# Kernel tuning notes

Measured on AMD Instinct MI355X. Metric: run time of the kernel, lower is better.

## Reference

```python
import jax, jax.numpy as jnp
import numpy as np

WH, WW = 7, 7
N = WH * WW
DIM = 384
HEADS = 12
NW = 64          # windows per image
B_ = 2048        # batch * NW


def _relative_position_index():
    ch, cw = np.meshgrid(np.arange(WH), np.arange(WW), indexing='ij')
    coords = np.stack([ch, cw]).reshape(2, -1)                      # [2, N]
    rel = coords[:, :, None] - coords[:, None, :]                   # [2, N, N]
    rel = rel.transpose(1, 2, 0)
    rel[:, :, 0] += WH - 1
    rel[:, :, 1] += WW - 1
    rel[:, :, 0] *= 2 * WW - 1
    return jnp.asarray(rel.sum(-1), dtype=jnp.int32)                # [N, N]


def setup_inputs() -> dict:
    key = jax.random.key(0)
    ks = jax.random.split(key, 7)
    return {
        'x': jax.random.normal(ks[0], (B_, N, DIM), dtype=jnp.float32),
        'qkv_w': jax.random.normal(ks[1], (3 * DIM, DIM), dtype=jnp.float32) * 0.02,
        'qkv_b': jax.random.normal(ks[2], (3 * DIM,), dtype=jnp.float32) * 0.02,
        'proj_w': jax.random.normal(ks[3], (DIM, DIM), dtype=jnp.float32) * 0.02,
        'proj_b': jax.random.normal(ks[4], (DIM,), dtype=jnp.float32) * 0.02,
        'bias_table': jax.random.normal(ks[5], ((2 * WH - 1) * (2 * WW - 1), HEADS), dtype=jnp.float32) * 0.02,
        'mask': jax.random.normal(ks[6], (NW, N, N), dtype=jnp.float32),
        'rel_idx': _relative_position_index(),
    }


def reference(x, qkv_w, qkv_b, proj_w, proj_b, bias_table, mask, rel_idx):
    B_, n, C = x.shape
    H = HEADS
    hd = C // H
    scale = hd ** (-0.5)

    qkv = x @ qkv_w.T + qkv_b                                        # [B_, N, 3C]
    qkv = qkv.reshape(B_, n, 3, H, hd).transpose(2, 0, 3, 1, 4)      # [3, B_, H, N, hd]
    q, k, v = qkv[0], qkv[1], qkv[2]

    attn = jnp.einsum('bhqd,bhkd->bhqk', q * scale, k)               # [B_, H, N, N]

    rpb = bias_table[rel_idx.reshape(-1)].reshape(n, n, H)           # gather [N, N, H]
    attn = attn + rpb.transpose(2, 0, 1)[None]                       # [B_, H, N, N]

    nW = mask.shape[0]
    attn = attn.reshape(B_ // nW, nW, H, n, n) + mask[None, :, None]
    attn = attn.reshape(B_, H, n, n)
    attn = jax.nn.softmax(attn, axis=-1)

    out = jnp.einsum('bhqk,bhkd->bhqd', attn, v)                     # [B_, H, N, hd]
    out = out.transpose(0, 2, 1, 3).reshape(B_, n, C)
    return out @ proj_w.T + proj_b
```

## Files before the change

kernel.cpp:

```cpp
#include <hip/hip_runtime.h>
#include <hip/hip_bf16.h>
#include <cstdint>
#include <cstddef>

#define NTOK 49
#define DIM 384
#define KDIM 384
#define HEADS 12
#define HD 32
#define BATCH 2048
#define MROWS (BATCH * NTOK)

typedef unsigned short u16;
typedef __bf16 bf16x8 __attribute__((ext_vector_type(8)));
typedef unsigned short u16x8 __attribute__((ext_vector_type(8)));
typedef float f32x4 __attribute__((ext_vector_type(4)));

__device__ __forceinline__ u16 f2b(float f) {
  union { float f; unsigned u; } v; v.f = f;
  unsigned r = v.u + 0x7fffu + ((v.u >> 16) & 1u);
  return (u16)(r >> 16);
}

__device__ __forceinline__ bf16x8 ld_bf8(const u16* p) {
  u16x8 u = *(const u16x8*)p;
  return __builtin_bit_cast(bf16x8, u);
}

__device__ __forceinline__ void gload_lds16(const void* g, void* l) {
  __builtin_amdgcn_global_load_lds(
      (const __attribute__((address_space(1))) unsigned*)g,
      (__attribute__((address_space(3))) unsigned*)l, 16, 0, 0);
}

__global__ __launch_bounds__(256) void k_prep(const float* __restrict__ x,
                                              u16* __restrict__ xb,
                                              const float* __restrict__ qkv_w,
                                              u16* __restrict__ wqkvb,
                                              const float* __restrict__ proj_w,
                                              u16* __restrict__ wprojb,
                                              const float* __restrict__ bias_table,
                                              const float* __restrict__ mask,
                                              const int* __restrict__ rel_idx,
                                              float* __restrict__ rpbm) {
  int blk = blockIdx.x;
  if (blk < 38208) {
    const float* in;
    u16* out;
    int i;
    if (blk < 37632) {
      in = x; out = xb; i = blk * 256 + threadIdx.x;
    } else if (blk < 38064) {
      in = qkv_w; out = wqkvb; i = (blk - 37632) * 256 + threadIdx.x;
    } else {
      in = proj_w; out = wprojb; i = (blk - 38064) * 256 + threadIdx.x;
    }
    float4 v = ((const float4*)in)[i];
    ushort4 o;
    o.x = f2b(v.x); o.y = f2b(v.y); o.z = f2b(v.z); o.w = f2b(v.w);
    ((ushort4*)out)[i] = o;
  } else {
    int idx = (blk - 38208) * 256 + threadIdx.x;
    int r  = idx & 3;
    int l  = (idx >> 2) & 63;
    int ni = (idx >> 8) & 3;
    int mi = (idx >> 10) & 3;
    int w  = (idx >> 12) & 63;
    int h  = idx >> 18;
    int row = mi * 16 + (l >> 4) * 4 + r;
    int col = ni * 16 + (l & 15);
    float v = -1e30f;
    if (row < NTOK && col < NTOK)
      v = bias_table[rel_idx[row * NTOK + col] * HEADS + h] +
          mask[(w * NTOK + row) * NTOK + col];
    rpbm[idx] = v;
  }
}

template <int OUT_BF16, int NCOLS, int NTN, int GD8>
__global__ __launch_bounds__(256) void k_gemm(const u16* __restrict__ A,
                                              const u16* __restrict__ B,
                                              const float* __restrict__ bias,
                                              void* __restrict__ Cv) {
  __shared__ u16 sh[24576];
  int bid = blockIdx.x;
  int tile = (bid & 7) * GD8 + (bid >> 3);
  int mt = tile / NTN, nt = tile - mt * NTN;
  long m0 = (long)mt * 128;
  int n0 = nt * 128;
  int tid = threadIdx.x;
  int lane = tid & 63, wid = tid >> 6;
  int wr = (wid >> 1) * 64, wc = (wid & 1) * 64;
  int c = lane & 15, g = lane >> 4;
  int gsw = (g ^ ((c >> 1) & 3)) * 8;

  int srow = wid * 16 + (lane >> 2);
  int scol = ((lane & 3) ^ ((lane >> 3) & 3)) * 8;
  const u16* gA = A + (m0 + srow) * (long)KDIM + scol;
  const u16* gB = B + (long)(n0 + srow) * KDIM + scol;
  int lrow = srow, lseg = (lane & 3) * 8;

  f32x4 acc[4][4] = {};

#define STAGE(BUF, KT)                                                         \
  {                                                                            \
    u16* As_ = sh + (BUF) * 8192;                                              \
    u16* Bs_ = As_ + 4096;                                                     \
    gload_lds16(gA + (KT), &As_[lrow * 32 + lseg]);                            \
    gload_lds16(gA + (KT) + 64L * KDIM, &As_[(lrow + 64) * 32 + lseg]);        \
    gload_lds16(gB + (KT), &Bs_[lrow * 32 + lseg]);                            \
    gload_lds16(gB + (KT) + 64L * KDIM, &Bs_[(lrow + 64) * 32 + lseg]);        \
  }

#define GITER(T, NV)                                                           \
  {                                                                            \
    asm volatile("s_waitcnt vmcnt(" #NV ")" ::: "memory");                     \
    __builtin_amdgcn_s_barrier();                                              \
    const u16* As = sh + ((T) % 3) * 8192;                                     \
    const u16* Bs = As + 4096;                                                 \
    bf16x8 af[4], bfr[4];                                                      \
    _Pragma("unroll") for (int i = 0; i < 4; ++i) {                            \
      af[i]  = ld_bf8(&As[(wr + i * 16 + c) * 32 + gsw]);                      \
      bfr[i] = ld_bf8(&Bs[(wc + i * 16 + c) * 32 + gsw]);                      \
    }                                                                          \
    asm volatile("s_waitcnt lgkmcnt(0)" ::: "memory");                         \
    __builtin_amdgcn_s_barrier();                                              \
    if ((T) + 3 < 12) STAGE((T) % 3, ((T) + 3) * 32);                          \
    __builtin_amdgcn_s_setprio(1);                                             \
    _Pragma("unroll") for (int mi = 0; mi < 4; ++mi)                           \
    _Pragma("unroll") for (int ni = 0; ni < 4; ++ni)                           \
        acc[mi][ni] = __builtin_amdgcn_mfma_f32_16x16x32_bf16(                 \
            af[mi], bfr[ni], acc[mi][ni], 0, 0, 0);                            \
    __builtin_amdgcn_s_setprio(0);                                             \
  }

  STAGE(0, 0);
  STAGE(1, 32);
  STAGE(2, 64);
  GITER(0, 8)  GITER(1, 8)  GITER(2, 8)  GITER(3, 8)
  GITER(4, 8)  GITER(5, 8)  GITER(6, 8)  GITER(7, 8)
  GITER(8, 8)  GITER(9, 8)  GITER(10, 4) GITER(11, 0)
#undef GITER
#undef STAGE

  if (OUT_BF16) {
    u16* C = (u16*)Cv;
#pragma unroll
    for (int mi = 0; mi < 4; ++mi)
#pragma unroll
      for (int ni = 0; ni < 4; ++ni) {
        int col = wc + ni * 16 + c;
        float bv = bias[n0 + col];
#pragma unroll
        for (int r = 0; r < 4; ++r) {
          int row = wr + mi * 16 + g * 4 + r;
          sh[row * 128 + col] = f2b(acc[mi][ni][r] + bv);
        }
      }
    __syncthreads();
#pragma unroll
    for (int rep = 0; rep < 8; ++rep) {
      int idx = rep * 2048 + tid * 8;
      int row = idx >> 7, col = idx & 127;
      *(u16x8*)(C + (m0 + row) * NCOLS + n0 + col) = *(const u16x8*)&sh[idx];
    }
  } else {
    float* C = (float*)Cv;
    float* shf = (float*)sh;
#pragma unroll
    for (int chunk = 0; chunk < 2; ++chunk) {
      __syncthreads();
      if ((wr >> 6) == chunk) {
#pragma unroll
        for (int mi = 0; mi < 4; ++mi)
#pragma unroll
          for (int ni = 0; ni < 4; ++ni) {
            int col = wc + ni * 16 + c;
            float bv = bias[n0 + col];
#pragma unroll
            for (int r = 0; r < 4; ++r) {
              int lr = mi * 16 + g * 4 + r;
              shf[lr * 128 + col] = acc[mi][ni][r] + bv;
            }
          }
      }
      __syncthreads();
#pragma unroll
      for (int rep = 0; rep < 8; ++rep) {
        int idx = rep * 1024 + tid * 4;
        int row = idx >> 7, col = idx & 127;
        *(float4*)(C + (m0 + chunk * 64 + row) * NCOLS + n0 + col) =
            *(const float4*)&shf[idx];
      }
    }
  }
}

__global__ __launch_bounds__(256) void k_attn(const u16* __restrict__ qkv,
                                              const float* __restrict__ rpbm,
                                              u16* __restrict__ attnout) {
  __shared__ u16 P_lds[4][64 * 64];
  __shared__ u16 vT_lds[4][32 * 64];
  int lane = threadIdx.x & 63, wid = threadIdx.x >> 6;
  int blk = blockIdx.x;
  int w = blk / 96;
  int rr = blk - w * 96;
  int j = rr / 3;
  int hb = rr - j * 3;
  int b = j * 64 + w;
  int h = hb * 4 + wid;
  const u16* base = qkv + (size_t)b * (NTOK * 1152);
  int c = lane & 15, g = lane >> 4;

  u16* vt = vT_lds[wid];
  {
    const u16* vbase = base + 2 * DIM + h * HD;
#pragma unroll
    for (int t = 0; t < 4; ++t) {
      int idx = t * 64 + lane;
      int jj = idx >> 2, d0 = (idx & 3) * 8;
      int jr = jj < NTOK ? jj : NTOK - 1;
      u16x8 vv = *(const u16x8*)(vbase + (size_t)jr * 1152 + d0);
#pragma unroll
      for (int dd = 0; dd < 8; ++dd) {
        int d = d0 + dd;
        int byte = (d * 128 + jj * 2) ^ ((d & 7) << 4);
        *(u16*)((char*)vt + byte) = (u16)vv[dd];
      }
    }
  }

  bf16x8 qa[4], kb[4];
#pragma unroll
  for (int mi = 0; mi < 4; ++mi) {
    int row = mi * 16 + c; if (row > NTOK - 1) row = NTOK - 1;
    qa[mi] = ld_bf8(base + (size_t)row * 1152 + h * HD + g * 8);
  }
#pragma unroll
  for (int ni = 0; ni < 4; ++ni) {
    int row = ni * 16 + c; if (row > NTOK - 1) row = NTOK - 1;
    kb[ni] = ld_bf8(base + (size_t)row * 1152 + DIM + h * HD + g * 8);
  }

  f32x4 s[4][4] = {};
#pragma unroll
  for (int mi = 0; mi < 4; ++mi)
#pragma unroll
    for (int ni = 0; ni < 4; ++ni)
      s[mi][ni] = __builtin_amdgcn_mfma_f32_16x16x32_bf16(qa[mi], kb[ni],
                                                          s[mi][ni], 0, 0, 0);

  const float scale = 0.17677669529663687f;
  const f32x4* rp = (const f32x4*)(rpbm + ((size_t)(h * 64 + w)) * 4096);
#pragma unroll
  for (int mi = 0; mi < 4; ++mi)
#pragma unroll
    for (int ni = 0; ni < 4; ++ni) {
      f32x4 rv = rp[(mi * 4 + ni) * 64 + lane];
#pragma unroll
      for (int r = 0; r < 4; ++r)
        s[mi][ni][r] = s[mi][ni][r] * scale + rv[r];
    }

#pragma unroll
  for (int mi = 0; mi < 4; ++mi)
#pragma unroll
    for (int r = 0; r < 4; ++r) {
      float mx = fmaxf(fmaxf(s[mi][0][r], s[mi][1][r]),
                       fmaxf(s[mi][2][r], s[mi][3][r]));
      mx = fmaxf(mx, __shfl_xor(mx, 1));
      mx = fmaxf(mx, __shfl_xor(mx, 2));
      mx = fmaxf(mx, __shfl_xor(mx, 4));
      mx = fmaxf(mx, __shfl_xor(mx, 8));
      float sum = 0.f;
#pragma unroll
      for (int ni = 0; ni < 4; ++ni) {
        float p = __expf(s[mi][ni][r] - mx);
        s[mi][ni][r] = p;
        sum += p;
      }
      sum += __shfl_xor(sum, 1);
      sum += __shfl_xor(sum, 2);
      sum += __shfl_xor(sum, 4);
      sum += __shfl_xor(sum, 8);
      float inv = __builtin_amdgcn_rcpf(sum);
#pragma unroll
      for (int ni = 0; ni < 4; ++ni) s[mi][ni][r] *= inv;
    }

  u16* pl = P_lds[wid];
#pragma unroll
  for (int mi = 0; mi < 4; ++mi)
#pragma unroll
    for (int ni = 0; ni < 4; ++ni) {
      int col = ni * 16 + c;
#pragma unroll
      for (int r = 0; r < 4; ++r) {
        int row = mi * 16 + g * 4 + r;
        int byte = (row * 128 + col * 2) ^ ((row & 7) << 4);
        *(u16*)((char*)pl + byte) = f2b(s[mi][ni][r]);
      }
    }
  asm volatile("s_waitcnt lgkmcnt(0)" ::: "memory");

  f32x4 o[4][2] = {};
#pragma unroll
  for (int ks = 0; ks < 2; ++ks) {
    bf16x8 vb[2];
#pragma unroll
    for (int n2 = 0; n2 < 2; ++n2) {
      int d = n2 * 16 + c;
      int byte = (d * 128 + ks * 64 + g * 16) ^ ((d & 7) << 4);
      vb[n2] = __builtin_bit_cast(bf16x8, *(const u16x8*)((const char*)vt + byte));
    }
#pragma unroll
    for (int mi = 0; mi < 4; ++mi) {
      int row = mi * 16 + c;
      int byte = (row * 128 + ks * 64 + g * 16) ^ ((row & 7) << 4);
      bf16x8 pa = __builtin_bit_cast(bf16x8, *(const u16x8*)((const char*)pl + byte));
#pragma unroll
      for (int n2 = 0; n2 < 2; ++n2)
        o[mi][n2] = __builtin_amdgcn_mfma_f32_16x16x32_bf16(pa, vb[n2],
                                                            o[mi][n2], 0, 0, 0);
    }
  }

  u16* obase = attnout + (size_t)b * (NTOK * DIM) + h * HD;
#pragma unroll
  for (int mi = 0; mi < 4; ++mi)
#pragma unroll
    for (int r = 0; r < 4; ++r) {
      int row = mi * 16 + g * 4 + r;
      if (row < NTOK) {
#pragma unroll
        for (int n2 = 0; n2 < 2; ++n2)
          obase[(size_t)row * DIM + n2 * 16 + c] = f2b(o[mi][n2][r]);
      }
    }
}

extern "C" void kernel_launch(void* const* d_in, const int* in_sizes, int n_in,
                              void* d_out, int out_size, void* d_ws, size_t ws_size,
                              hipStream_t stream) {
  const float* x       = (const float*)d_in[0];
  const float* qkv_w   = (const float*)d_in[1];
  const float* qkv_b   = (const float*)d_in[2];
  const float* proj_w  = (const float*)d_in[3];
  const float* proj_b  = (const float*)d_in[4];
  const float* bias_tb = (const float*)d_in[5];
  const float* mask    = (const float*)d_in[6];
  const int*   rel_idx = (const int*)d_in[7];
  float* out = (float*)d_out;

  char* ws = (char*)d_ws;
  u16*   xb      = (u16*)(ws + 0);
  u16*   wqkvb   = (u16*)(ws + 77070336);
  u16*   wprojb  = (u16*)(ws + 77955072);
  float* rpbm    = (float*)(ws + 78249984);
  u16*   qkv     = (u16*)(ws + 90832896);
  u16*   attnout = (u16*)(ws + 322043904);

  k_prep<<<50496, 256, 0, stream>>>(x, xb, qkv_w, wqkvb, proj_w, wprojb,
                                    bias_tb, mask, rel_idx, rpbm);

  k_gemm<1, 1152, 9, 882><<<7056, 256, 0, stream>>>(xb, wqkvb, qkv_b, (void*)qkv);

  k_attn<<<6144, 256, 0, stream>>>(qkv, rpbm, attnout);

  k_gemm<0, 384, 3, 294><<<2352, 256, 0, stream>>>(attnout, wprojb, proj_b,
                                                   (void*)out);

  (void)in_sizes; (void)n_in; (void)out_size; (void)ws_size;
}
```

Baseline: 350.3 us.

## Enlarge GEMM tiles to 256x128 with 512 threads and software-pipelined fragment reads

Both GEMMs now use a 256x128 output tile computed by 8 waves (512 threads), so each B tile loaded into LDS is reused across twice as many rows, halving the number of blocks. The main loop is also restructured so the MFMA cluster for the current k-step runs before the wait and barrier, and LDS fragments for the next step are prefetched right after staging. This removes one barrier per iteration and overlaps LDS reads with compute. In exchange it uses more LDS per block (72 KB) and fewer blocks, which may lower occupancy and worsen tail balance. The epilogue indexing is adapted to the taller tile.

```diff
diff --git a/kernel.cpp b/kernel.cpp
--- a/kernel.cpp
+++ b/kernel.cpp
@@ -78,15 +78,15 @@
 }
 
 template <int OUT_BF16, int NCOLS, int NTN, int GD8>
-__global__ __launch_bounds__(256) void k_gemm(const u16* __restrict__ A,
-                                              const u16* __restrict__ B,
-                                              const float* __restrict__ bias,
-                                              void* __restrict__ Cv) {
-  __shared__ u16 sh[24576];
+__global__ __launch_bounds__(512, 4) void k_gemm256(const u16* __restrict__ A,
+                                                    const u16* __restrict__ B,
+                                                    const float* __restrict__ bias,
+                                                    void* __restrict__ Cv) {
+  __shared__ u16 sh[36864];
   int bid = blockIdx.x;
   int tile = (bid & 7) * GD8 + (bid >> 3);
   int mt = tile / NTN, nt = tile - mt * NTN;
-  long m0 = (long)mt * 128;
+  long m0 = (long)mt * 256;
   int n0 = nt * 128;
   int tid = threadIdx.x;
   int lane = tid & 63, wid = tid >> 6;
@@ -101,47 +101,62 @@
   int lrow = srow, lseg = (lane & 3) * 8;
 
   f32x4 acc[4][4] = {};
-
-#define STAGE(BUF, KT)                                                         \
+  bf16x8 af[4], bfr[4];
+
+#define STAGE256(BUF, KT)                                                      \
   {                                                                            \
-    u16* As_ = sh + (BUF) * 8192;                                              \
-    u16* Bs_ = As_ + 4096;                                                     \
+    u16* As_ = sh + (BUF) * 12288;                                             \
+    u16* Bs_ = As_ + 8192;                                                     \
     gload_lds16(gA + (KT), &As_[lrow * 32 + lseg]);                            \
-    gload_lds16(gA + (KT) + 64L * KDIM, &As_[(lrow + 64) * 32 + lseg]);        \
+    gload_lds16(gA + (KT) + 128L * KDIM, &As_[(lrow + 128) * 32 + lseg]);      \
     gload_lds16(gB + (KT), &Bs_[lrow * 32 + lseg]);                            \
-    gload_lds16(gB + (KT) + 64L * KDIM, &Bs_[(lrow + 64) * 32 + lseg]);        \
-  }
-
-#define GITER(T, NV)                                                           \
+  }
+
+#define FRAGREAD(BUF)                                                          \
   {                                                                            \
-    asm volatile("s_waitcnt vmcnt(" #NV ")" ::: "memory");                     \
-    __builtin_amdgcn_s_barrier();                                              \
-    const u16* As = sh + ((T) % 3) * 8192;                                     \
-    const u16* Bs = As + 4096;                                                 \
-    bf16x8 af[4], bfr[4];                                                      \
+    const u16* As = sh + (BUF) * 12288;                                        \
+    const u16* Bs = As + 8192;                                                 \
     _Pragma("unroll") for (int i = 0; i < 4; ++i) {                            \
       af[i]  = ld_bf8(&As[(wr + i * 16 + c) * 32 + gsw]);                      \
       bfr[i] = ld_bf8(&Bs[(wc + i * 16 + c) * 32 + gsw]);                      \
     }                                                                          \
-    asm volatile("s_waitcnt lgkmcnt(0)" ::: "memory");                         \
+  }
+
+#define MFMA_CL                                                                \
+  __builtin_amdgcn_s_setprio(1);                                               \
+  _Pragma("unroll") for (int mi = 0; mi < 4; ++mi)                             \
+  _Pragma("unroll") for (int ni = 0; ni < 4; ++ni)                             \
+      acc[mi][ni] = __builtin_amdgcn_mfma_f32_16x16x32_bf16(                   \
+          af[mi], bfr[ni], acc[mi][ni], 0, 0, 0);                              \
+  __builtin_amdgcn_s_setprio(0);
+
+#define GITER(T, NV)                                                           \
+  {                                                                            \
+    MFMA_CL;                                                                   \
+    asm volatile("s_waitcnt vmcnt(" #NV ")" ::: "memory");                     \
     __builtin_amdgcn_s_barrier();                                              \
-    if ((T) + 3 < 12) STAGE((T) % 3, ((T) + 3) * 32);                          \
-    __builtin_amdgcn_s_setprio(1);                                             \
-    _Pragma("unroll") for (int mi = 0; mi < 4; ++mi)                           \
-    _Pragma("unroll") for (int ni = 0; ni < 4; ++ni)                           \
-        acc[mi][ni] = __builtin_amdgcn_mfma_f32_16x16x32_bf16(                 \
-            af[mi], bfr[ni], acc[mi][ni], 0, 0, 0);                            \
-    __builtin_amdgcn_s_setprio(0);                                             \
-  }
-
-  STAGE(0, 0);
-  STAGE(1, 32);
-  STAGE(2, 64);
-  GITER(0, 8)  GITER(1, 8)  GITER(2, 8)  GITER(3, 8)
-  GITER(4, 8)  GITER(5, 8)  GITER(6, 8)  GITER(7, 8)
-  GITER(8, 8)  GITER(9, 8)  GITER(10, 4) GITER(11, 0)
+    __builtin_amdgcn_sched_barrier(0);                                         \
+    if ((T) + 3 < 12) STAGE256((T) % 3, ((T) + 3) * 32);                       \
+    FRAGREAD(((T) + 1) % 3);                                                   \
+  }
+
+  STAGE256(0, 0);
+  STAGE256(1, 32);
+  STAGE256(2, 64);
+  asm volatile("s_waitcnt vmcnt(6)" ::: "memory");
+  __builtin_amdgcn_s_barrier();
+  __builtin_amdgcn_sched_barrier(0);
+  FRAGREAD(0);
+
+  GITER(0, 3)  GITER(1, 3)  GITER(2, 3)  GITER(3, 3)
+  GITER(4, 3)  GITER(5, 3)  GITER(6, 3)  GITER(7, 3)
+  GITER(8, 3)  GITER(9, 3)  GITER(10, 0)
+  { MFMA_CL; }
+  __builtin_amdgcn_s_barrier();
 #undef GITER
-#undef STAGE
+#undef MFMA_CL
+#undef FRAGREAD
+#undef STAGE256
 
   if (OUT_BF16) {
     u16* C = (u16*)Cv;
@@ -160,7 +175,7 @@
     __syncthreads();
 #pragma unroll
     for (int rep = 0; rep < 8; ++rep) {
-      int idx = rep * 2048 + tid * 8;
+      int idx = rep * 4096 + tid * 8;
       int row = idx >> 7, col = idx & 127;
       *(u16x8*)(C + (m0 + row) * NCOLS + n0 + col) = *(const u16x8*)&sh[idx];
     }
@@ -170,7 +185,7 @@
 #pragma unroll
     for (int chunk = 0; chunk < 2; ++chunk) {
       __syncthreads();
-      if ((wr >> 6) == chunk) {
+      if ((wid >> 2) == chunk) {
 #pragma unroll
         for (int mi = 0; mi < 4; ++mi)
 #pragma unroll
@@ -179,7 +194,7 @@
             float bv = bias[n0 + col];
 #pragma unroll
             for (int r = 0; r < 4; ++r) {
-              int lr = mi * 16 + g * 4 + r;
+              int lr = ((wid >> 1) & 1) * 64 + mi * 16 + g * 4 + r;
               shf[lr * 128 + col] = acc[mi][ni][r] + bv;
             }
           }
@@ -187,9 +202,9 @@
       __syncthreads();
 #pragma unroll
       for (int rep = 0; rep < 8; ++rep) {
-        int idx = rep * 1024 + tid * 4;
+        int idx = rep * 2048 + tid * 4;
         int row = idx >> 7, col = idx & 127;
-        *(float4*)(C + (m0 + chunk * 64 + row) * NCOLS + n0 + col) =
+        *(float4*)(C + (m0 + chunk * 128 + row) * NCOLS + n0 + col) =
             *(const float4*)&shf[idx];
       }
     }
@@ -363,12 +378,13 @@
   k_prep<<<50496, 256, 0, stream>>>(x, xb, qkv_w, wqkvb, proj_w, wprojb,
                                     bias_tb, mask, rel_idx, rpbm);
 
-  k_gemm<1, 1152, 9, 882><<<7056, 256, 0, stream>>>(xb, wqkvb, qkv_b, (void*)qkv);
+  k_gemm256<1, 1152, 9, 441><<<3528, 512, 0, stream>>>(xb, wqkvb, qkv_b,
+                                                       (void*)qkv);
 
   k_attn<<<6144, 256, 0, stream>>>(qkv, rpbm, attnout);
 
-  k_gemm<0, 384, 3, 294><<<2352, 256, 0, stream>>>(attnout, wprojb, proj_b,
-                                                   (void*)out);
+  k_gemm256<0, 384, 3, 147><<<1176, 512, 0, stream>>>(attnout, wprojb, proj_b,
+                                                      (void*)out);
 
   (void)in_sizes; (void)n_in; (void)out_size; (void)ws_size;
 }
```

New measurement: 342.3 us. 2.3% less time.
